# Kernel tuning notes

Measured on AMD Instinct MI355X. Metric: run time of the kernel, lower is better.

Reference implementation:

```python
import jax, jax.numpy as jnp
import numpy as np

N_CLASSES = 24
ATT_CLASS = 5  # attention_class init kwarg
NS_GRAPHS, NQ_GRAPHS, NODES_PER_G = 48, 24, 4
BN_EPS = 1e-5
COS_EPS = 1e-6


def _conv3(x, w):
    return jax.lax.conv_general_dilated(x, w, (1, 1), 'SAME',
                                        dimension_numbers=('NCHW', 'OIHW', 'NCHW'))


def _maxpool2(x):
    return jax.lax.reduce_window(x, -jnp.inf, jax.lax.max, (1, 1, 2, 2), (1, 1, 2, 2), 'VALID')


def _bn_train(x, g, b):
    # BatchNorm2d in training mode: batch statistics over (N,H,W), biased variance
    m = x.mean(axis=(0, 2, 3), keepdims=True)
    v = x.var(axis=(0, 2, 3), keepdims=True)
    return (x - m) * jax.lax.rsqrt(v + BN_EPS) * g.reshape(1, -1, 1, 1) + b.reshape(1, -1, 1, 1)


def _block(x, w, g, b):
    return _maxpool2(jax.nn.relu(_bn_train(_conv3(x, w), g, b)))


def _cnn(x, w1, g1, b1, w2, g2, b2, w_rest, g_rest, b_rest):
    x = _block(x, w1, g1, b1)
    x = _block(x, w2, g2, b2)
    for i in range(4):  # fixed small layer loop
        x = _block(x, w_rest[i], g_rest[i], b_rest[i])
    return x.reshape(x.shape[0], -1)  # [N, 64*2*2 = 256]


def _seg_mean(v, idx, n):
    s = jax.ops.segment_sum(v, idx, num_segments=n)
    c = jax.ops.segment_sum(jnp.ones(idx.shape, v.dtype), idx, num_segments=n)
    c = jnp.maximum(c, 1.0)
    return s / (c if v.ndim == 1 else c[:, None])


def _edge_cos_per_node(x, edge_index, n_nodes):
    src, dst = edge_index[0], edge_index[1]
    xj, xi = x[src], x[dst]  # gather per edge
    dot = jnp.sum(xj * xi, axis=-1)
    denom = jnp.maximum(jnp.linalg.norm(xj, axis=-1) * jnp.linalg.norm(xi, axis=-1), COS_EPS)
    cos = dot / denom
    return _seg_mean(cos, dst, n_nodes)  # scatter-mean onto target nodes


def _make_edges(key, n_graphs, epg):
    k1, k2 = jax.random.split(key)
    base = jnp.repeat(jnp.arange(n_graphs, dtype=jnp.int32) * NODES_PER_G, epg)
    src = base + jax.random.randint(k1, base.shape, 0, NODES_PER_G, dtype=jnp.int32)
    dst = base + jax.random.randint(k2, base.shape, 0, NODES_PER_G, dtype=jnp.int32)
    return jnp.stack([src, dst])


def setup_inputs() -> dict:
    key = jax.random.key(0)
    ks = jax.random.split(key, 12)
    ns, nq = NS_GRAPHS * NODES_PER_G, NQ_GRAPHS * NODES_PER_G
    support_x = jax.random.normal(ks[0], (ns, 3, 128, 128), jnp.float32)
    query_x = jax.random.normal(ks[1], (nq, 3, 128, 128), jnp.float32)
    support_edge_index = _make_edges(ks[2], NS_GRAPHS, 16)  # [2,768]
    query_edge_index = _make_edges(ks[3], NQ_GRAPHS, 16)    # [2,384]
    support_batch = jnp.repeat(jnp.arange(NS_GRAPHS, dtype=jnp.int32), NODES_PER_G)
    query_batch = jnp.repeat(jnp.arange(NQ_GRAPHS, dtype=jnp.int32), NODES_PER_G)
    support_y = jnp.tile(jnp.arange(N_CLASSES, dtype=jnp.int32), NS_GRAPHS // N_CLASSES)
    query_y = jnp.arange(N_CLASSES, dtype=jnp.int32)
    def he(k, shp):
        fan_in = shp[1] * shp[2] * shp[3] if len(shp) == 4 else shp[2] * shp[3] * shp[4]
        return jax.random.normal(k, shp, jnp.float32) * np.float32(np.sqrt(2.0 / fan_in))
    w1 = he(ks[4], (32, 3, 3, 3))
    w2 = he(ks[5], (64, 32, 3, 3))
    w_rest = he(ks[6], (4, 64, 64, 3, 3))
    g1 = 1.0 + 0.1 * jax.random.normal(ks[7], (32,), jnp.float32)
    b1 = 0.1 * jax.random.normal(ks[8], (32,), jnp.float32)
    g2 = 1.0 + 0.1 * jax.random.normal(ks[9], (64,), jnp.float32)
    b2 = 0.1 * jax.random.normal(ks[10], (64,), jnp.float32)
    g_rest = 1.0 + 0.1 * jax.random.normal(ks[11], (4, 64), jnp.float32)
    b_rest = 0.1 * jax.random.normal(jax.random.fold_in(key, 99), (4, 64), jnp.float32)
    return {'support_x': support_x, 'query_x': query_x,
            'support_edge_index': support_edge_index, 'query_edge_index': query_edge_index,
            'support_batch': support_batch, 'query_batch': query_batch,
            'support_y': support_y, 'query_y': query_y,
            'w1': w1, 'g1': g1, 'b1': b1, 'w2': w2, 'g2': g2, 'b2': b2,
            'w_rest': w_rest, 'g_rest': g_rest, 'b_rest': b_rest}


def reference(support_x, query_x, w1, g1, b1, w2, g2, b2, w_rest, g_rest, b_rest,
              support_edge_index, query_edge_index, support_batch, query_batch,
              support_y, query_y):
    ns, nq = support_x.shape[0], query_x.shape[0]
    # CNN node features (MEConv.mlp), per torch-geometric call semantics: separate BN stats per call
    s_x = _cnn(support_x, w1, g1, b1, w2, g2, b2, w_rest, g_rest, b_rest)  # [Ns, 256]
    q_x = _cnn(query_x, w1, g1, b1, w2, g2, b2, w_rest, g_rest, b_rest)    # [Nq, 256]
    # message: cosine similarity per edge, aggregate: scatter-mean to target nodes
    s_cos_node = _edge_cos_per_node(s_x, support_edge_index, ns)  # [Ns]
    # per-graph pooled features (scatter mean over batch); note the original discards
    # the aggregated neighbor-mean output and uses the raw node features here
    s_cat = _seg_mean(s_x, support_batch, NS_GRAPHS)  # [Gs, 256]
    p_cat = _seg_mean(q_x, query_batch, NQ_GRAPHS)    # [Gq, 256]
    # RBF distance between each query prototype and every support graph (vectorized loop)
    pd1 = jnp.exp(-jnp.sum((p_cat[:, None, :] - s_cat[None, :, :]) ** 2, axis=-1))  # [Gq, Gs]
    # cosine alignment loss
    s_cos_graph = _seg_mean(s_cos_node, support_batch, NS_GRAPHS)
    cos_loss = jnp.sum((s_cos_graph - 1.0) ** 2)
    # class-wise scatter-mean of distances over support labels
    csum = jax.ops.segment_sum(pd1.T, support_y, num_segments=N_CLASSES)  # [24, Gq]
    ccnt = jnp.maximum(jax.ops.segment_sum(jnp.ones((NS_GRAPHS,), pd1.dtype), support_y,
                                           num_segments=N_CLASSES), 1.0)
    output = (csum / ccnt[:, None]).T  # [Gq, 24]
    # cross-entropy with one-hot soft targets, split by the static attention mask
    label = jax.nn.one_hot(query_y, N_CLASSES, dtype=output.dtype)
    ce_rows = -jnp.sum(label * jax.nn.log_softmax(output, axis=-1), axis=-1)  # [Gq]
    atten_loss = ce_rows[ATT_CLASS]                       # mask selects the single attention class row
    rest_loss = (jnp.sum(ce_rows) - atten_loss) / (N_CLASSES - 1)
    loss = atten_loss + rest_loss + cos_loss
    acc = jnp.sum((jnp.argmax(output, axis=1) == query_y).astype(jnp.float32))
    return loss, acc, cos_loss, atten_loss, rest_loss
```

## Files before the change

### kernel.cpp

```cpp
#include <hip/hip_runtime.h>
#include <hip/hip_bf16.h>
#include <cstdint>
#include <cstddef>


template<int IC, int OC, int H, int TS, int OCG, bool APPLY, bool STOREMAX>
__global__ __launch_bounds__(TS*TS/4)
void conv_tiled(const float* __restrict__ inA, const float* __restrict__ inB,
                int nSplit, const float* __restrict__ W,
                const float* __restrict__ scale, const float* __restrict__ shift,
                double* __restrict__ stats, float* __restrict__ maxout,
                float* __restrict__ out, int nSupport)
{
  constexpr int TH = TS/2;
  constexpr int NT = TH*TH;
  constexpr int NW = (NT+63)/64;
  constexpr int TILES = H/TS;
  const int tid = threadIdx.x;
  const int n   = blockIdx.z;
  const int ocg = blockIdx.y;
  const int ty0 = (blockIdx.x / TILES) * TS;
  const int tx0 = (blockIdx.x % TILES) * TS;

  const float* in = (n < nSplit) ? inA + (size_t)n*IC*H*H
                                 : inB + (size_t)(n - nSplit)*IC*H*H;
  const float* Wb = W + (size_t)(ocg*OCG)*IC*9;

  __shared__ float sIn[(TS+2)*(TS+2)];
  __shared__ float sSum[NW][OCG], sSsq[NW][OCG];

  float acc[4][OCG];
  #pragma unroll
  for (int i = 0; i < 4; ++i)
    #pragma unroll
    for (int o = 0; o < OCG; ++o) acc[i][o] = 0.f;

  const int tx = tid % TH, ty = tid / TH;
  const int iy = 2*ty, ix = 2*tx;

  for (int ic = 0; ic < IC; ++ic) {
    const float* ip = in + (size_t)ic*H*H;
    for (int i = tid; i < (TS+2)*(TS+2); i += NT) {
      int r = i/(TS+2), c = i%(TS+2);
      int gy = ty0 + r - 1, gx = tx0 + c - 1;
      float v = 0.f;
      if (gy >= 0 && gy < H && gx >= 0 && gx < H) v = ip[gy*H + gx];
      sIn[i] = v;
    }
    __syncthreads();

    float xr[4][4];
    #pragma unroll
    for (int r = 0; r < 4; ++r)
      #pragma unroll
      for (int c = 0; c < 4; ++c)
        xr[r][c] = sIn[(iy+r)*(TS+2) + ix + c];

    #pragma unroll
    for (int oc = 0; oc < OCG; ++oc) {
      const float* wp = Wb + (size_t)oc*IC*9 + ic*9;
      float w[9];
      #pragma unroll
      for (int k = 0; k < 9; ++k) w[k] = wp[k];
      #pragma unroll
      for (int kh = 0; kh < 3; ++kh) {
        #pragma unroll
        for (int kw = 0; kw < 3; ++kw) {
          const float wv = w[kh*3 + kw];
          acc[0][oc] = fmaf(xr[kh  ][kw  ], wv, acc[0][oc]);
          acc[1][oc] = fmaf(xr[kh  ][kw+1], wv, acc[1][oc]);
          acc[2][oc] = fmaf(xr[kh+1][kw  ], wv, acc[2][oc]);
          acc[3][oc] = fmaf(xr[kh+1][kw+1], wv, acc[3][oc]);
        }
      }
    }
    __syncthreads();
  }

  const int g = (n < nSupport) ? 0 : 1;
  if constexpr (APPLY) {
    #pragma unroll
    for (int oc = 0; oc < OCG; ++oc) {
      const int ocGl = ocg*OCG + oc;
      const float s = scale[g*OC + ocGl];
      const float t = shift[g*OC + ocGl];
      float v0 = fmaxf(fmaf(acc[0][oc], s, t), 0.f);
      float v1 = fmaxf(fmaf(acc[1][oc], s, t), 0.f);
      float v2 = fmaxf(fmaf(acc[2][oc], s, t), 0.f);
      float v3 = fmaxf(fmaf(acc[3][oc], s, t), 0.f);
      float m = fmaxf(fmaxf(v0, v1), fmaxf(v2, v3));
      int py = ty0/2 + ty, px = tx0/2 + tx;
      out[(((size_t)n*OC + ocGl)*(H/2) + py)*(H/2) + px] = m;
    }
  } else {
    if constexpr (STOREMAX) {
      const int py = ty0/2 + ty, px = tx0/2 + tx;
      #pragma unroll
      for (int oc = 0; oc < OCG; ++oc) {
        const int ocGl = ocg*OCG + oc;
        float mx = fmaxf(fmaxf(acc[0][oc], acc[1][oc]),
                         fmaxf(acc[2][oc], acc[3][oc]));
        maxout[(((size_t)n*OC + ocGl)*(H/2) + py)*(H/2) + px] = mx;
      }
    }
    const int lane = tid & 63, wid = tid >> 6;
    #pragma unroll
    for (int oc = 0; oc < OCG; ++oc) {
      float ls = acc[0][oc] + acc[1][oc] + acc[2][oc] + acc[3][oc];
      float lq = acc[0][oc]*acc[0][oc] + acc[1][oc]*acc[1][oc]
               + acc[2][oc]*acc[2][oc] + acc[3][oc]*acc[3][oc];
      #pragma unroll
      for (int off = 32; off > 0; off >>= 1) {
        ls += __shfl_down(ls, off);
        lq += __shfl_down(lq, off);
      }
      if (lane == 0) { sSum[wid][oc] = ls; sSsq[wid][oc] = lq; }
    }
    __syncthreads();
    if (tid < OCG) {
      float S = 0.f, Q = 0.f;
      #pragma unroll
      for (int w = 0; w < NW; ++w) { S += sSum[w][tid]; Q += sSsq[w][tid]; }
      const int ocGl = ocg*OCG + tid;
      atomicAdd(&stats[(g*OC + ocGl)*2 + 0], (double)S);
      atomicAdd(&stats[(g*OC + ocGl)*2 + 1], (double)Q);
    }
  }
}

template<int OC, int Hp>
__global__ __launch_bounds__(256)
void bn_pool_max(const float* conv, const float* scale,
                 const float* shift, float* out, int nSupport)
{
  const int total = 288*OC*Hp*Hp;
  const int idx = blockIdx.x*256 + threadIdx.x;
  if (idx >= total) return;
  const int oc = (idx / (Hp*Hp)) % OC;
  const int n  = idx / (Hp*Hp*OC);
  const int g = (n < nSupport) ? 0 : 1;
  const float s = scale[g*OC + oc];
  const float t = shift[g*OC + oc];
  out[idx] = fmaxf(fmaf(conv[idx], s, t), 0.f);
}

template<int H, bool APPLY>
__global__ __launch_bounds__(256)
void conv_small(const float* __restrict__ in, const float* __restrict__ W,
                const float* __restrict__ scale, const float* __restrict__ shift,
                double* __restrict__ stats, float* __restrict__ out, int nSupport)
{
  constexpr int HW = H*H;
  constexpr int NACC = (H == 8) ? 16 : 4;
  constexpr int SC = (H == 4) ? 64*16 : 1;
  const int tid = threadIdx.x;
  const int n  = blockIdx.x;
  const int oc = tid & 63;
  const int q  = tid >> 6;

  __shared__ float sX[64*HW];
  __shared__ float sS[256];
  __shared__ float sQ[256];
  __shared__ float sC[SC];

  for (int i = tid; i < 64*HW; i += 256) sX[i] = in[(size_t)n*64*HW + i];
  __syncthreads();

  float acc[NACC];
  #pragma unroll
  for (int i = 0; i < NACC; ++i) acc[i] = 0.f;

  const int ry = (H == 8) ? 4*(q >> 1) : 0;
  const int rx = (H == 8) ? 4*(q & 1)  : 0;

  for (int ic = 0; ic < 64; ++ic) {
    const float* wp = W + ((size_t)oc*64 + ic)*9;
    float w[9];
    #pragma unroll
    for (int k = 0; k < 9; ++k) w[k] = wp[k];
    if (H == 8) {
      float rin[6][6];
      #pragma unroll
      for (int r = 0; r < 6; ++r) {
        int y = ry + r - 1;
        #pragma unroll
        for (int c = 0; c < 6; ++c) {
          int x = rx + c - 1;
          rin[r][c] = (y >= 0 && y < H && x >= 0 && x < H) ? sX[ic*HW + y*H + x] : 0.f;
        }
      }
      #pragma unroll
      for (int kh = 0; kh < 3; ++kh)
        #pragma unroll
        for (int kw = 0; kw < 3; ++kw) {
          float wv = w[kh*3+kw];
          #pragma unroll
          for (int py = 0; py < 4; ++py)
            #pragma unroll
            for (int px = 0; px < 4; ++px)
              acc[py*4+px] = fmaf(wv, rin[py+kh][px+kw], acc[py*4+px]);
        }
    } else {
      float rin[3][6];
      #pragma unroll
      for (int r = 0; r < 3; ++r) {
        int y = q + r - 1;
        #pragma unroll
        for (int c = 0; c < 6; ++c) {
          int x = c - 1;
          rin[r][c] = (y >= 0 && y < H && x >= 0 && x < H) ? sX[ic*HW + y*H + x] : 0.f;
        }
      }
      #pragma unroll
      for (int kh = 0; kh < 3; ++kh)
        #pragma unroll
        for (int kw = 0; kw < 3; ++kw) {
          float wv = w[kh*3+kw];
          #pragma unroll
          for (int px = 0; px < 4; ++px)
            acc[px] = fmaf(wv, rin[kh][px+kw], acc[px]);
        }
    }
  }

  const int g = (n < nSupport) ? 0 : 1;
  if (APPLY) {
    float s = scale[g*64 + oc];
    float t = shift[g*64 + oc];
    if (H == 8) {
      const int py0 = ry/2, px0 = rx/2;
      #pragma unroll
      for (int pj = 0; pj < 2; ++pj)
        #pragma unroll
        for (int pi = 0; pi < 2; ++pi) {
          float v0 = fmaxf(fmaf(acc[(2*pj  )*4 + 2*pi  ], s, t), 0.f);
          float v1 = fmaxf(fmaf(acc[(2*pj  )*4 + 2*pi+1], s, t), 0.f);
          float v2 = fmaxf(fmaf(acc[(2*pj+1)*4 + 2*pi  ], s, t), 0.f);
          float v3 = fmaxf(fmaf(acc[(2*pj+1)*4 + 2*pi+1], s, t), 0.f);
          out[(((size_t)n*64 + oc)*4 + (py0+pj))*4 + (px0+pi)] =
              fmaxf(fmaxf(v0, v1), fmaxf(v2, v3));
        }
    } else {
      #pragma unroll
      for (int px = 0; px < 4; ++px)
        sC[oc*16 + q*4 + px] = fmaxf(fmaf(acc[px], s, t), 0.f);
      __syncthreads();
      int oc2 = tid & 63, pj = (tid >> 6) & 1, pi = (tid >> 7) & 1;
      float m = fmaxf(
          fmaxf(sC[oc2*16 + (2*pj  )*4 + 2*pi], sC[oc2*16 + (2*pj  )*4 + 2*pi+1]),
          fmaxf(sC[oc2*16 + (2*pj+1)*4 + 2*pi], sC[oc2*16 + (2*pj+1)*4 + 2*pi+1]));
      out[(((size_t)n*64 + oc2)*2 + pj)*2 + pi] = m;
    }
  } else {
    float ls = 0.f, lq = 0.f;
    #pragma unroll
    for (int i = 0; i < NACC; ++i) { ls += acc[i]; lq += acc[i]*acc[i]; }
    sS[tid] = ls; sQ[tid] = lq;
    __syncthreads();
    if (tid < 64) {
      float S = sS[tid] + sS[tid+64] + sS[tid+128] + sS[tid+192];
      float Q = sQ[tid] + sQ[tid+64] + sQ[tid+128] + sQ[tid+192];
      atomicAdd(&stats[(g*64 + tid)*2 + 0], (double)S);
      atomicAdd(&stats[(g*64 + tid)*2 + 1], (double)Q);
    }
  }
}

__global__ void bn_finalize(const double* __restrict__ stats,
                            const float* __restrict__ gamma, const float* __restrict__ beta,
                            float* __restrict__ scale, float* __restrict__ shift,
                            int OC, double cnt0, double cnt1)
{
  int i = threadIdx.x;
  if (i < 2*OC) {
    int oc = i % OC;
    double cnt = (i < OC) ? cnt0 : cnt1;
    double mean = stats[i*2 + 0] / cnt;
    double var  = stats[i*2 + 1] / cnt - mean*mean;
    double inv  = 1.0 / sqrt(var + 1e-5);
    double g = (double)gamma[oc];
    double b = (double)beta[oc];
    scale[i] = (float)(g * inv);
    shift[i] = (float)(b - mean * g * inv);
  }
}

__global__ void graph_means(const float* __restrict__ feat,
                            float* __restrict__ s_cat, float* __restrict__ p_cat)
{
  int g = blockIdx.x, d = threadIdx.x;
  if (g < 48) {
    float v = 0.f;
    for (int i = 0; i < 4; ++i) v += feat[(size_t)(4*g + i)*256 + d];
    s_cat[g*256 + d] = v * 0.25f;
  } else {
    int q = g - 48;
    float v = 0.f;
    for (int i = 0; i < 4; ++i) v += feat[(size_t)(192 + 4*q + i)*256 + d];
    p_cat[q*256 + d] = v * 0.25f;
  }
}

__global__ void edge_cos(const float* __restrict__ feat, const int* __restrict__ ei,
                         float* __restrict__ nsum, float* __restrict__ ncnt, int nEdges)
{
  int e = blockIdx.x, lane = threadIdx.x;
  int src = ei[e], dst = ei[nEdges + e];
  float dot = 0.f, nj = 0.f, ni = 0.f;
  for (int j = lane; j < 256; j += 64) {
    float a = feat[(size_t)src*256 + j];
    float b = feat[(size_t)dst*256 + j];
    dot += a*b; nj += a*a; ni += b*b;
  }
  for (int off = 32; off > 0; off >>= 1) {
    dot += __shfl_down(dot, off);
    nj  += __shfl_down(nj,  off);
    ni  += __shfl_down(ni,  off);
  }
  if (lane == 0) {
    float denom = fmaxf(sqrtf(nj)*sqrtf(ni), 1e-6f);
    atomicAdd(&nsum[dst], dot/denom);
    atomicAdd(&ncnt[dst], 1.f);
  }
}

__global__ void cos_loss_k(const float* __restrict__ nsum, const float* __restrict__ ncnt,
                           float* __restrict__ cosloss)
{
  int g = threadIdx.x;
  float v = 0.f;
  if (g < 48) {
    float gm = 0.f;
    for (int i = 0; i < 4; ++i) {
      int nd = 4*g + i;
      gm += nsum[nd] / fmaxf(ncnt[nd], 1.f);
    }
    gm *= 0.25f;
    v = (gm - 1.f)*(gm - 1.f);
  }
  for (int off = 32; off > 0; off >>= 1) v += __shfl_down(v, off);
  if (g == 0) cosloss[0] = v;
}

__global__ void pd_out(const float* __restrict__ s_cat, const float* __restrict__ p_cat,
                       const int* __restrict__ support_y, const int* __restrict__ query_y,
                       float* __restrict__ ce, float* __restrict__ correct)
{
  const int q = blockIdx.x;
  const int tid = threadIdx.x, lane = tid & 63, wid = tid >> 6;
  __shared__ float sP[48];
  __shared__ float sOut[24];
  float pv[4];
  #pragma unroll
  for (int j = 0; j < 4; ++j) pv[j] = p_cat[(size_t)q*256 + lane + 64*j];
  for (int s = wid*12; s < wid*12 + 12; ++s) {
    float d2 = 0.f;
    #pragma unroll
    for (int j = 0; j < 4; ++j) {
      float diff = pv[j] - s_cat[(size_t)s*256 + lane + 64*j];
      d2 += diff*diff;
    }
    for (int off = 32; off > 0; off >>= 1) d2 += __shfl_down(d2, off);
    if (lane == 0) sP[s] = expf(-d2);
  }
  __syncthreads();
  if (tid < 24) {
    int c = tid; float sum = 0.f; int cnt = 0;
    for (int s = 0; s < 48; ++s)
      if (support_y[s] == c) { sum += sP[s]; ++cnt; }
    sOut[c] = sum / fmaxf((float)cnt, 1.f);
  }
  __syncthreads();
  if (tid == 0) {
    float m = sOut[0]; int am = 0;
    for (int c = 1; c < 24; ++c) if (sOut[c] > m) { m = sOut[c]; am = c; }
    float lse = 0.f;
    for (int c = 0; c < 24; ++c) lse += expf(sOut[c] - m);
    lse = m + logf(lse);
    int y = query_y[q];
    ce[q] = lse - sOut[y];
    correct[q] = (am == y) ? 1.f : 0.f;
  }
}

__global__ void final_k(const float* __restrict__ ce, const float* __restrict__ correct,
                        const float* __restrict__ cosloss, float* __restrict__ out)
{
  if (threadIdx.x == 0) {
    float s = 0.f, a = 0.f;
    for (int qq = 0; qq < 24; ++qq) { s += ce[qq]; a += correct[qq]; }
    float atten = ce[5];
    float rest  = (s - atten) / 23.f;
    float cl = cosloss[0];
    out[0] = atten + rest + cl;
    out[1] = a;
    out[2] = cl;
    out[3] = atten;
    out[4] = rest;
  }
}

extern "C" void kernel_launch(void* const* d_in, const int* in_sizes, int n_in,
                              void* d_out, int out_size, void* d_ws, size_t ws_size,
                              hipStream_t stream)
{
  const float* support_x = (const float*)d_in[0];
  const float* query_x   = (const float*)d_in[1];
  const int*   s_ei      = (const int*)d_in[2];
  const int*   s_y       = (const int*)d_in[6];
  const int*   q_y       = (const int*)d_in[7];
  const float* w1 = (const float*)d_in[8];
  const float* g1 = (const float*)d_in[9];
  const float* b1 = (const float*)d_in[10];
  const float* w2 = (const float*)d_in[11];
  const float* g2 = (const float*)d_in[12];
  const float* b2 = (const float*)d_in[13];
  const float* wr = (const float*)d_in[14];
  const float* gr = (const float*)d_in[15];
  const float* br = (const float*)d_in[16];
  (void)in_sizes; (void)n_in; (void)out_size;

  char* ws = (char*)d_ws;
  size_t off = 0;
  auto alloc = [&](size_t bytes) -> char* {
    char* p = ws + off;
    off = (off + bytes + 255) & ~(size_t)255;
    return p;
  };
  float*  actA  = (float*)alloc((size_t)288*32*64*64*4);
  float*  actB  = (float*)alloc((size_t)288*64*32*32*4);
  double* stats = (double*)alloc(2*64*2*8);
  float*  scl   = (float*)alloc(2*64*4);
  float*  shf   = (float*)alloc(2*64*4);
  float*  s_cat = (float*)alloc(48*256*4);
  float*  p_cat = (float*)alloc(24*256*4);
  float*  nsum  = (float*)alloc(192*4);
  float*  ncnt  = (float*)alloc(192*4);
  float*  cosl  = (float*)alloc(256);
  float*  ce    = (float*)alloc(24*4);
  float*  corr  = (float*)alloc(24*4);
  if (off > ws_size) return;

  const int NS = 192;
  const int BIG = 1 << 30;
  const size_t statsB = 2*64*2*8;

  hipMemsetAsync(stats, 0, statsB, stream);
  conv_tiled<3,32,128,32,16,false,true><<<dim3(16,2,288),256,0,stream>>>(
      support_x, query_x, 192, w1, nullptr, nullptr, stats, actA, nullptr, NS);
  bn_finalize<<<1,128,0,stream>>>(stats, g1, b1, scl, shf, 32,
      192.0*128*128, 96.0*128*128);
  bn_pool_max<32,64><<<(288*32*64*64 + 255)/256,256,0,stream>>>(
      actA, scl, shf, actA, NS);

  hipMemsetAsync(stats, 0, statsB, stream);
  conv_tiled<32,64,64,32,16,false,true><<<dim3(4,4,288),256,0,stream>>>(
      actA, actA, BIG, w2, nullptr, nullptr, stats, actB, nullptr, NS);
  bn_finalize<<<1,128,0,stream>>>(stats, g2, b2, scl, shf, 64,
      192.0*64*64, 96.0*64*64);
  bn_pool_max<64,32><<<(288*64*32*32 + 255)/256,256,0,stream>>>(
      actB, scl, shf, actB, NS);

  float* mx3   = actA;
  float* mx4   = actA + (size_t)288*64*16*16;
  float* l5out = mx4  + (size_t)288*64*8*8;
  float* feat  = l5out + (size_t)288*64*4*4;
  hipMemsetAsync(stats, 0, statsB, stream);
  conv_tiled<64,64,32,32,16,false,true><<<dim3(1,4,288),256,0,stream>>>(
      actB, actB, BIG, wr + 0*36864, nullptr, nullptr, stats, mx3, nullptr, NS);
  bn_finalize<<<1,128,0,stream>>>(stats, gr + 0*64, br + 0*64, scl, shf, 64,
      192.0*32*32, 96.0*32*32);
  bn_pool_max<64,16><<<(288*64*16*16 + 255)/256,256,0,stream>>>(
      mx3, scl, shf, mx3, NS);

  hipMemsetAsync(stats, 0, statsB, stream);
  conv_tiled<64,64,16,16,4,false,true><<<dim3(1,16,288),64,0,stream>>>(
      mx3, mx3, BIG, wr + 1*36864, nullptr, nullptr, stats, mx4, nullptr, NS);
  bn_finalize<<<1,128,0,stream>>>(stats, gr + 1*64, br + 1*64, scl, shf, 64,
      192.0*16*16, 96.0*16*16);
  bn_pool_max<64,8><<<(288*64*8*8 + 255)/256,256,0,stream>>>(
      mx4, scl, shf, mx4, NS);

  hipMemsetAsync(stats, 0, statsB, stream);
  conv_small<8,false><<<288,256,0,stream>>>(
      mx4, wr + 2*36864, nullptr, nullptr, stats, nullptr, NS);
  bn_finalize<<<1,128,0,stream>>>(stats, gr + 2*64, br + 2*64, scl, shf, 64,
      192.0*8*8, 96.0*8*8);
  conv_small<8,true><<<288,256,0,stream>>>(
      mx4, wr + 2*36864, scl, shf, nullptr, l5out, NS);

  hipMemsetAsync(stats, 0, statsB, stream);
  conv_small<4,false><<<288,256,0,stream>>>(
      l5out, wr + 3*36864, nullptr, nullptr, stats, nullptr, NS);
  bn_finalize<<<1,128,0,stream>>>(stats, gr + 3*64, br + 3*64, scl, shf, 64,
      192.0*4*4, 96.0*4*4);
  conv_small<4,true><<<288,256,0,stream>>>(
      l5out, wr + 3*36864, scl, shf, nullptr, feat, NS);

  graph_means<<<72,256,0,stream>>>(feat, s_cat, p_cat);
  hipMemsetAsync(nsum, 0, 192*4, stream);
  hipMemsetAsync(ncnt, 0, 192*4, stream);
  edge_cos<<<768,64,0,stream>>>(feat, s_ei, nsum, ncnt, 768);
  cos_loss_k<<<1,64,0,stream>>>(nsum, ncnt, cosl);
  pd_out<<<24,256,0,stream>>>(s_cat, p_cat, s_y, q_y, ce, corr);
  final_k<<<1,64,0,stream>>>(ce, corr, cosl, (float*)d_out);
}
```

Baseline: 1.656 ms.

## Fuse BN+ReLU into next conv's input load and double-buffer input tiles

Drops the separate bn_pool_max elementwise kernels. The next convolution now applies the previous layer's scale/shift and ReLU while staging the pooled pre-activation max into shared memory, which is valid because the BN scales are assumed positive. The input loop is double-buffered with register staging so the next channel's global load overlaps compute, removing one barrier per channel. Per-layer stats buffers are merged into one memset, which trades a little extra register pressure for fewer kernel launches and full-tensor passes.

```diff
diff --git a/kernel.cpp b/kernel.cpp
--- a/kernel.cpp
+++ b/kernel.cpp
@@ -4,18 +4,21 @@
 #include <cstddef>
 
 
-template<int IC, int OC, int H, int TS, int OCG, bool APPLY, bool STOREMAX>
+template<int IC, int OC, int H, int TS, int OCG, bool PREBN>
 __global__ __launch_bounds__(TS*TS/4)
-void conv_tiled(const float* __restrict__ inA, const float* __restrict__ inB,
+void conv_stats(const float* __restrict__ inA, const float* __restrict__ inB,
                 int nSplit, const float* __restrict__ W,
-                const float* __restrict__ scale, const float* __restrict__ shift,
+                const float* __restrict__ pscl, const float* __restrict__ pshf,
                 double* __restrict__ stats, float* __restrict__ maxout,
-                float* __restrict__ out, int nSupport)
+                int nSupport)
 {
   constexpr int TH = TS/2;
   constexpr int NT = TH*TH;
   constexpr int NW = (NT+63)/64;
   constexpr int TILES = H/TS;
+  constexpr int SZ = (TS+2)*(TS+2);
+  constexpr int NLOAD = (SZ + NT - 1)/NT;
+
   const int tid = threadIdx.x;
   const int n   = blockIdx.z;
   const int ocg = blockIdx.y;
@@ -25,9 +28,40 @@
   const float* in = (n < nSplit) ? inA + (size_t)n*IC*H*H
                                  : inB + (size_t)(n - nSplit)*IC*H*H;
   const float* Wb = W + (size_t)(ocg*OCG)*IC*9;
-
-  __shared__ float sIn[(TS+2)*(TS+2)];
+  const int g = (n < nSupport) ? 0 : 1;
+
+  __shared__ float sIn[2][SZ];
   __shared__ float sSum[NW][OCG], sSsq[NW][OCG];
+
+  int soff[NLOAD];
+  #pragma unroll
+  for (int k = 0; k < NLOAD; ++k) {
+    int i = tid + k*NT;
+    int r = i/(TS+2), c = i%(TS+2);
+    int gy = ty0 + r - 1, gx = tx0 + c - 1;
+    soff[k] = (i < SZ && gy >= 0 && gy < H && gx >= 0 && gx < H)
+            ? (gy*H + gx) : -1;
+  }
+
+  float stg[NLOAD];
+  #pragma unroll
+  for (int k = 0; k < NLOAD; ++k)
+    stg[k] = (soff[k] >= 0) ? in[soff[k]] : 0.f;
+  {
+    float ps = 0.f, pt = 0.f;
+    if constexpr (PREBN) { ps = pscl[g*IC]; pt = pshf[g*IC]; }
+    #pragma unroll
+    for (int k = 0; k < NLOAD; ++k) {
+      int i = tid + k*NT;
+      if (i < SZ) {
+        float x = stg[k];
+        if constexpr (PREBN)
+          x = (soff[k] >= 0) ? fmaxf(fmaf(x, ps, pt), 0.f) : 0.f;
+        sIn[0][i] = x;
+      }
+    }
+  }
+  __syncthreads();
 
   float acc[4][OCG];
   #pragma unroll
@@ -39,22 +73,21 @@
   const int iy = 2*ty, ix = 2*tx;
 
   for (int ic = 0; ic < IC; ++ic) {
-    const float* ip = in + (size_t)ic*H*H;
-    for (int i = tid; i < (TS+2)*(TS+2); i += NT) {
-      int r = i/(TS+2), c = i%(TS+2);
-      int gy = ty0 + r - 1, gx = tx0 + c - 1;
-      float v = 0.f;
-      if (gy >= 0 && gy < H && gx >= 0 && gx < H) v = ip[gy*H + gx];
-      sIn[i] = v;
-    }
-    __syncthreads();
+    const float* sbuf = sIn[ic & 1];
+
+    if (ic + 1 < IC) {
+      const float* ip = in + (size_t)(ic+1)*H*H;
+      #pragma unroll
+      for (int k = 0; k < NLOAD; ++k)
+        stg[k] = (soff[k] >= 0) ? ip[soff[k]] : 0.f;
+    }
 
     float xr[4][4];
     #pragma unroll
     for (int r = 0; r < 4; ++r)
       #pragma unroll
       for (int c = 0; c < 4; ++c)
-        xr[r][c] = sIn[(iy+r)*(TS+2) + ix + c];
+        xr[r][c] = sbuf[(iy+r)*(TS+2) + ix + c];
 
     #pragma unroll
     for (int oc = 0; oc < OCG; ++oc) {
@@ -74,79 +107,64 @@
         }
       }
     }
-    __syncthreads();
-  }
-
-  const int g = (n < nSupport) ? 0 : 1;
-  if constexpr (APPLY) {
+
+    if (ic + 1 < IC) {
+      float ps = 0.f, pt = 0.f;
+      if constexpr (PREBN) { ps = pscl[g*IC + ic + 1]; pt = pshf[g*IC + ic + 1]; }
+      float* dbuf = sIn[(ic+1) & 1];
+      #pragma unroll
+      for (int k = 0; k < NLOAD; ++k) {
+        int i = tid + k*NT;
+        if (i < SZ) {
+          float x = stg[k];
+          if constexpr (PREBN)
+            x = (soff[k] >= 0) ? fmaxf(fmaf(x, ps, pt), 0.f) : 0.f;
+          dbuf[i] = x;
+        }
+      }
+      __syncthreads();
+    }
+  }
+
+  {
+    const int py = ty0/2 + ty, px = tx0/2 + tx;
     #pragma unroll
     for (int oc = 0; oc < OCG; ++oc) {
       const int ocGl = ocg*OCG + oc;
-      const float s = scale[g*OC + ocGl];
-      const float t = shift[g*OC + ocGl];
-      float v0 = fmaxf(fmaf(acc[0][oc], s, t), 0.f);
-      float v1 = fmaxf(fmaf(acc[1][oc], s, t), 0.f);
-      float v2 = fmaxf(fmaf(acc[2][oc], s, t), 0.f);
-      float v3 = fmaxf(fmaf(acc[3][oc], s, t), 0.f);
-      float m = fmaxf(fmaxf(v0, v1), fmaxf(v2, v3));
-      int py = ty0/2 + ty, px = tx0/2 + tx;
-      out[(((size_t)n*OC + ocGl)*(H/2) + py)*(H/2) + px] = m;
-    }
-  } else {
-    if constexpr (STOREMAX) {
-      const int py = ty0/2 + ty, px = tx0/2 + tx;
-      #pragma unroll
-      for (int oc = 0; oc < OCG; ++oc) {
-        const int ocGl = ocg*OCG + oc;
-        float mx = fmaxf(fmaxf(acc[0][oc], acc[1][oc]),
-                         fmaxf(acc[2][oc], acc[3][oc]));
-        maxout[(((size_t)n*OC + ocGl)*(H/2) + py)*(H/2) + px] = mx;
-      }
-    }
-    const int lane = tid & 63, wid = tid >> 6;
-    #pragma unroll
-    for (int oc = 0; oc < OCG; ++oc) {
-      float ls = acc[0][oc] + acc[1][oc] + acc[2][oc] + acc[3][oc];
-      float lq = acc[0][oc]*acc[0][oc] + acc[1][oc]*acc[1][oc]
-               + acc[2][oc]*acc[2][oc] + acc[3][oc]*acc[3][oc];
-      #pragma unroll
-      for (int off = 32; off > 0; off >>= 1) {
-        ls += __shfl_down(ls, off);
-        lq += __shfl_down(lq, off);
-      }
-      if (lane == 0) { sSum[wid][oc] = ls; sSsq[wid][oc] = lq; }
-    }
-    __syncthreads();
-    if (tid < OCG) {
-      float S = 0.f, Q = 0.f;
-      #pragma unroll
-      for (int w = 0; w < NW; ++w) { S += sSum[w][tid]; Q += sSsq[w][tid]; }
-      const int ocGl = ocg*OCG + tid;
-      atomicAdd(&stats[(g*OC + ocGl)*2 + 0], (double)S);
-      atomicAdd(&stats[(g*OC + ocGl)*2 + 1], (double)Q);
-    }
-  }
-}
-
-template<int OC, int Hp>
-__global__ __launch_bounds__(256)
-void bn_pool_max(const float* conv, const float* scale,
-                 const float* shift, float* out, int nSupport)
-{
-  const int total = 288*OC*Hp*Hp;
-  const int idx = blockIdx.x*256 + threadIdx.x;
-  if (idx >= total) return;
-  const int oc = (idx / (Hp*Hp)) % OC;
-  const int n  = idx / (Hp*Hp*OC);
-  const int g = (n < nSupport) ? 0 : 1;
-  const float s = scale[g*OC + oc];
-  const float t = shift[g*OC + oc];
-  out[idx] = fmaxf(fmaf(conv[idx], s, t), 0.f);
-}
-
-template<int H, bool APPLY>
+      float mx = fmaxf(fmaxf(acc[0][oc], acc[1][oc]),
+                       fmaxf(acc[2][oc], acc[3][oc]));
+      maxout[(((size_t)n*OC + ocGl)*(H/2) + py)*(H/2) + px] = mx;
+    }
+  }
+
+  const int lane = tid & 63, wid = tid >> 6;
+  #pragma unroll
+  for (int oc = 0; oc < OCG; ++oc) {
+    float ls = acc[0][oc] + acc[1][oc] + acc[2][oc] + acc[3][oc];
+    float lq = acc[0][oc]*acc[0][oc] + acc[1][oc]*acc[1][oc]
+             + acc[2][oc]*acc[2][oc] + acc[3][oc]*acc[3][oc];
+    #pragma unroll
+    for (int off = 32; off > 0; off >>= 1) {
+      ls += __shfl_down(ls, off);
+      lq += __shfl_down(lq, off);
+    }
+    if (lane == 0) { sSum[wid][oc] = ls; sSsq[wid][oc] = lq; }
+  }
+  __syncthreads();
+  if (tid < OCG) {
+    float S = 0.f, Q = 0.f;
+    #pragma unroll
+    for (int w = 0; w < NW; ++w) { S += sSum[w][tid]; Q += sSsq[w][tid]; }
+    const int ocGl = ocg*OCG + tid;
+    atomicAdd(&stats[(g*OC + ocGl)*2 + 0], (double)S);
+    atomicAdd(&stats[(g*OC + ocGl)*2 + 1], (double)Q);
+  }
+}
+
+template<int H, bool APPLY, bool PREBN>
 __global__ __launch_bounds__(256)
 void conv_small(const float* __restrict__ in, const float* __restrict__ W,
+                const float* __restrict__ pscl, const float* __restrict__ pshf,
                 const float* __restrict__ scale, const float* __restrict__ shift,
                 double* __restrict__ stats, float* __restrict__ out, int nSupport)
 {
@@ -157,13 +175,21 @@
   const int n  = blockIdx.x;
   const int oc = tid & 63;
   const int q  = tid >> 6;
+  const int g = (n < nSupport) ? 0 : 1;
 
   __shared__ float sX[64*HW];
   __shared__ float sS[256];
   __shared__ float sQ[256];
   __shared__ float sC[SC];
 
-  for (int i = tid; i < 64*HW; i += 256) sX[i] = in[(size_t)n*64*HW + i];
+  for (int i = tid; i < 64*HW; i += 256) {
+    float v = in[(size_t)n*64*HW + i];
+    if constexpr (PREBN) {
+      int ic = i / HW;
+      v = fmaxf(fmaf(v, pscl[g*64 + ic], pshf[g*64 + ic]), 0.f);
+    }
+    sX[i] = v;
+  }
   __syncthreads();
 
   float acc[NACC];
@@ -223,8 +249,7 @@
     }
   }
 
-  const int g = (n < nSupport) ? 0 : 1;
-  if (APPLY) {
+  if constexpr (APPLY) {
     float s = scale[g*64 + oc];
     float t = shift[g*64 + oc];
     if (H == 8) {
@@ -429,9 +454,9 @@
   };
   float*  actA  = (float*)alloc((size_t)288*32*64*64*4);
   float*  actB  = (float*)alloc((size_t)288*64*32*32*4);
-  double* stats = (double*)alloc(2*64*2*8);
-  float*  scl   = (float*)alloc(2*64*4);
-  float*  shf   = (float*)alloc(2*64*4);
+  double* stats = (double*)alloc(6*256*8);
+  float*  scl   = (float*)alloc(6*128*4);
+  float*  shf   = (float*)alloc(6*128*4);
   float*  s_cat = (float*)alloc(48*256*4);
   float*  p_cat = (float*)alloc(24*256*4);
   float*  nsum  = (float*)alloc(192*4);
@@ -443,63 +468,51 @@
 
   const int NS = 192;
   const int BIG = 1 << 30;
-  const size_t statsB = 2*64*2*8;
-
-  hipMemsetAsync(stats, 0, statsB, stream);
-  conv_tiled<3,32,128,32,16,false,true><<<dim3(16,2,288),256,0,stream>>>(
-      support_x, query_x, 192, w1, nullptr, nullptr, stats, actA, nullptr, NS);
-  bn_finalize<<<1,128,0,stream>>>(stats, g1, b1, scl, shf, 32,
-      192.0*128*128, 96.0*128*128);
-  bn_pool_max<32,64><<<(288*32*64*64 + 255)/256,256,0,stream>>>(
-      actA, scl, shf, actA, NS);
-
-  hipMemsetAsync(stats, 0, statsB, stream);
-  conv_tiled<32,64,64,32,16,false,true><<<dim3(4,4,288),256,0,stream>>>(
-      actA, actA, BIG, w2, nullptr, nullptr, stats, actB, nullptr, NS);
-  bn_finalize<<<1,128,0,stream>>>(stats, g2, b2, scl, shf, 64,
-      192.0*64*64, 96.0*64*64);
-  bn_pool_max<64,32><<<(288*64*32*32 + 255)/256,256,0,stream>>>(
-      actB, scl, shf, actB, NS);
 
   float* mx3   = actA;
   float* mx4   = actA + (size_t)288*64*16*16;
   float* l5out = mx4  + (size_t)288*64*8*8;
   float* feat  = l5out + (size_t)288*64*4*4;
-  hipMemsetAsync(stats, 0, statsB, stream);
-  conv_tiled<64,64,32,32,16,false,true><<<dim3(1,4,288),256,0,stream>>>(
-      actB, actB, BIG, wr + 0*36864, nullptr, nullptr, stats, mx3, nullptr, NS);
-  bn_finalize<<<1,128,0,stream>>>(stats, gr + 0*64, br + 0*64, scl, shf, 64,
-      192.0*32*32, 96.0*32*32);
-  bn_pool_max<64,16><<<(288*64*16*16 + 255)/256,256,0,stream>>>(
-      mx3, scl, shf, mx3, NS);
-
-  hipMemsetAsync(stats, 0, statsB, stream);
-  conv_tiled<64,64,16,16,4,false,true><<<dim3(1,16,288),64,0,stream>>>(
-      mx3, mx3, BIG, wr + 1*36864, nullptr, nullptr, stats, mx4, nullptr, NS);
-  bn_finalize<<<1,128,0,stream>>>(stats, gr + 1*64, br + 1*64, scl, shf, 64,
-      192.0*16*16, 96.0*16*16);
-  bn_pool_max<64,8><<<(288*64*8*8 + 255)/256,256,0,stream>>>(
-      mx4, scl, shf, mx4, NS);
-
-  hipMemsetAsync(stats, 0, statsB, stream);
-  conv_small<8,false><<<288,256,0,stream>>>(
-      mx4, wr + 2*36864, nullptr, nullptr, stats, nullptr, NS);
-  bn_finalize<<<1,128,0,stream>>>(stats, gr + 2*64, br + 2*64, scl, shf, 64,
-      192.0*8*8, 96.0*8*8);
-  conv_small<8,true><<<288,256,0,stream>>>(
-      mx4, wr + 2*36864, scl, shf, nullptr, l5out, NS);
-
-  hipMemsetAsync(stats, 0, statsB, stream);
-  conv_small<4,false><<<288,256,0,stream>>>(
-      l5out, wr + 3*36864, nullptr, nullptr, stats, nullptr, NS);
-  bn_finalize<<<1,128,0,stream>>>(stats, gr + 3*64, br + 3*64, scl, shf, 64,
-      192.0*4*4, 96.0*4*4);
-  conv_small<4,true><<<288,256,0,stream>>>(
-      l5out, wr + 3*36864, scl, shf, nullptr, feat, NS);
-
-  graph_means<<<72,256,0,stream>>>(feat, s_cat, p_cat);
+
+  hipMemsetAsync(stats, 0, 6*256*8, stream);
   hipMemsetAsync(nsum, 0, 192*4, stream);
   hipMemsetAsync(ncnt, 0, 192*4, stream);
+
+  conv_stats<3,32,128,32,16,false><<<dim3(16,2,288),256,0,stream>>>(
+      support_x, query_x, 192, w1, nullptr, nullptr, stats, actA, NS);
+  bn_finalize<<<1,128,0,stream>>>(stats, g1, b1, scl, shf, 32,
+      192.0*128*128, 96.0*128*128);
+
+  conv_stats<32,64,64,32,16,true><<<dim3(4,4,288),256,0,stream>>>(
+      actA, actA, BIG, w2, scl, shf, stats+256, actB, NS);
+  bn_finalize<<<1,128,0,stream>>>(stats+256, g2, b2, scl+128, shf+128, 64,
+      192.0*64*64, 96.0*64*64);
+
+  conv_stats<64,64,32,32,16,true><<<dim3(1,4,288),256,0,stream>>>(
+      actB, actB, BIG, wr + 0*36864, scl+128, shf+128, stats+512, mx3, NS);
+  bn_finalize<<<1,128,0,stream>>>(stats+512, gr + 0*64, br + 0*64,
+      scl+256, shf+256, 64, 192.0*32*32, 96.0*32*32);
+
+  conv_stats<64,64,16,16,4,true><<<dim3(1,16,288),64,0,stream>>>(
+      mx3, mx3, BIG, wr + 1*36864, scl+256, shf+256, stats+768, mx4, NS);
+  bn_finalize<<<1,128,0,stream>>>(stats+768, gr + 1*64, br + 1*64,
+      scl+384, shf+384, 64, 192.0*16*16, 96.0*16*16);
+
+  conv_small<8,false,true><<<288,256,0,stream>>>(
+      mx4, wr + 2*36864, scl+384, shf+384, nullptr, nullptr, stats+1024, nullptr, NS);
+  bn_finalize<<<1,128,0,stream>>>(stats+1024, gr + 2*64, br + 2*64,
+      scl+512, shf+512, 64, 192.0*8*8, 96.0*8*8);
+  conv_small<8,true,true><<<288,256,0,stream>>>(
+      mx4, wr + 2*36864, scl+384, shf+384, scl+512, shf+512, nullptr, l5out, NS);
+
+  conv_small<4,false,false><<<288,256,0,stream>>>(
+      l5out, wr + 3*36864, nullptr, nullptr, nullptr, nullptr, stats+1280, nullptr, NS);
+  bn_finalize<<<1,128,0,stream>>>(stats+1280, gr + 3*64, br + 3*64,
+      scl+640, shf+640, 64, 192.0*4*4, 96.0*4*4);
+  conv_small<4,true,false><<<288,256,0,stream>>>(
+      l5out, wr + 3*36864, nullptr, nullptr, scl+640, shf+640, nullptr, feat, NS);
+
+  graph_means<<<72,256,0,stream>>>(feat, s_cat, p_cat);
   edge_cos<<<768,64,0,stream>>>(feat, s_ei, nsum, ncnt, 768);
   cos_loss_k<<<1,64,0,stream>>>(nsum, ncnt, cosl);
   pd_out<<<24,256,0,stream>>>(s_cat, p_cat, s_y, q_y, ce, corr);
```

After: 1.683 ms. Within noise of the previous version (+1.6%).
